# Kernel tuning notes

Hardware: AMD Instinct MI355X
Metric: run time of the kernel (lower is better)

## Reference

```python
import jax, jax.numpy as jnp
import numpy as np

K_NN = 4  # hard-coded k in get_graph_feature(x, k=4)


def _conv1(h, Wm, s, b):
    # 1x1 conv1d + folded-BN (scale/shift) + ReLU
    return jax.nn.relu(jnp.einsum('oc,bcn->bon', Wm, h) * s[:, None] + b[:, None])


def _conv2(h, Wm, s, b):
    # 1x1 conv2d + folded-BN + ReLU
    return jax.nn.relu(jnp.einsum('oc,bcnk->bonk', Wm, h) * s[:, None, None] + b[:, None, None])


def _forward(x, W_dup, s_dup, b_dup, W_c1, s_c1, b_c1,
             W2a, s2a, b2a, W2b, s2b, b2b, W2c, s2c, b2c,
             W3a, s3a, b3a, W3b, s3b, b3b, W4a, bias4a, W4b, bias4b):
    B = x.shape[0]
    h = _conv1(x, W_dup, s_dup, b_dup)           # (B,256,1024)
    h = h.reshape(B, 128, 2048)                  # duplicate points: (B,128,2048)
    h = _conv1(h, W_c1, s_c1, b_c1)              # (B,64,2048)
    g = jnp.max(h, axis=2, keepdims=True)        # max_pool1d over all 2048 -> (B,64,1)
    # knn on 64-d features: pairwise = -||xi-xj||^2, topk picks nearest (self included)
    xx = jnp.sum(h * h, axis=1, keepdims=True)   # (B,1,P)
    inner = -2.0 * jnp.einsum('bcn,bcm->bnm', h, h)
    pd = -xx - inner - jnp.swapaxes(xx, 1, 2)    # (B,P,P)
    idx = jax.lax.top_k(pd, K_NN)[1]             # (B,P,k)
    xt = jnp.swapaxes(h, 1, 2)                   # (B,P,C)
    nb = xt[jnp.arange(B)[:, None, None], idx]   # gather neighbors: (B,P,k,C)
    ctr = xt[:, :, None, :]
    feat = jnp.concatenate([nb - ctr, jnp.broadcast_to(ctr, nb.shape)], axis=-1)  # (B,P,k,2C)
    feat = jnp.transpose(feat, (0, 3, 1, 2))     # (B,128,P,k)
    feat = _conv2(feat, W2a, s2a, b2a)
    feat = _conv2(feat, W2b, s2b, b2b)
    feat = _conv2(feat, W2c, s2c, b2c)           # (B,64,P,k)
    local = jnp.max(feat, axis=3)                # max over k -> (B,64,P)
    g = _conv1(g, W3a, s3a, b3a)
    g = _conv1(g, W3b, s3b, b3b)                 # (B,128,1)
    final = jnp.concatenate([local, jnp.broadcast_to(g, (B, 128, local.shape[2]))], axis=1)  # (B,192,P)
    h4 = jax.nn.relu(jnp.einsum('oc,bcn->bon', W4a, final) + bias4a[:, None])  # (B,256,P)
    out = jnp.einsum('oc,bcn->bon', W4b, h4) + bias4b[:, None]                 # (B,3,P)
    return out


def setup_inputs() -> dict:
    key = jax.random.key(0)
    ks = list(jax.random.split(key, 30))
    W = lambda k, o, c: jax.random.normal(k, (o, c), jnp.float32) * 0.05
    sc = lambda k, c: 1.0 + 0.1 * jax.random.normal(k, (c,), jnp.float32)
    bs = lambda k, c: 0.1 * jax.random.normal(k, (c,), jnp.float32)
    return {
        'search_keypoint': jax.random.normal(ks[0], (8, 128, 1024), jnp.float32),
        'W_dup': W(ks[1], 256, 128), 's_dup': sc(ks[2], 256), 'b_dup': bs(ks[3], 256),
        'W_c1': W(ks[4], 64, 128), 's_c1': sc(ks[5], 64), 'b_c1': bs(ks[6], 64),
        'W2a': W(ks[7], 64, 128), 's2a': sc(ks[8], 64), 'b2a': bs(ks[9], 64),
        'W2b': W(ks[10], 64, 64), 's2b': sc(ks[11], 64), 'b2b': bs(ks[12], 64),
        'W2c': W(ks[13], 64, 64), 's2c': sc(ks[14], 64), 'b2c': bs(ks[15], 64),
        'W3a': W(ks[16], 128, 64), 's3a': sc(ks[17], 128), 'b3a': bs(ks[18], 128),
        'W3b': W(ks[19], 128, 128), 's3b': sc(ks[20], 128), 'b3b': bs(ks[21], 128),
        'W4a': W(ks[22], 256, 192), 'bias4a': bs(ks[23], 256),
        'W4b': W(ks[24], 3, 256), 'bias4b': bs(ks[25], 3),
    }


def reference(search_keypoint, W_dup, s_dup, b_dup, W_c1, s_c1, b_c1,
              W2a, s2a, b2a, W2b, s2b, b2b, W2c, s2c, b2c,
              W3a, s3a, b3a, W3b, s3b, b3b, W4a, bias4a, W4b, bias4b):
    return _forward(search_keypoint, W_dup, s_dup, b_dup, W_c1, s_c1, b_c1,
                    W2a, s2a, b2a, W2b, s2b, b2b, W2c, s2c, b2c,
                    W3a, s3a, b3a, W3b, s3b, b3b, W4a, bias4a, W4b, bias4b)
```

## Files before the change

kernel.cpp:

```cpp
#include <hip/hip_runtime.h>
#include <float.h>

typedef __attribute__((ext_vector_type(8))) short short8;
typedef __attribute__((ext_vector_type(4))) float f32x4;
typedef unsigned short u16;
typedef unsigned long long u64;

static constexpr size_t OFF_W     = 0;
static constexpr size_t OFF_YZ    = 131072;
static constexpr size_t OFF_Zf    = 1179648;
static constexpr size_t OFF_FEATR = 2228224;
static constexpr size_t OFF_FIN   = 6422528;
static constexpr size_t OFF_XX    = 9568256;
static constexpr size_t OFF_G     = 9584640;
static constexpr size_t OFF_G3BS  = 9617408;
static constexpr size_t WS_FLOATS = 9652736;

static constexpr size_t WO_DUP = 0;
static constexpr size_t WO_C1  = 32768;
static constexpr size_t WO_2A  = 40960;
static constexpr size_t WO_2B  = 49152;
static constexpr size_t WO_2C  = 53248;
static constexpr size_t WO_4A  = 57344;

__device__ __forceinline__ void gl_lds16(const void* g, void* l) {
    __builtin_amdgcn_global_load_lds(
        (const __attribute__((address_space(1))) void*)g,
        (__attribute__((address_space(3))) void*)l, 16, 0, 0);
}

__device__ __forceinline__ u16 f2bf(float x) {
    union { float f; unsigned int u; } v; v.f = x;
    unsigned int r = v.u + 0x7fffu + ((v.u >> 16) & 1u);
    return (u16)(r >> 16);
}
__device__ __forceinline__ float bf2f(u16 h) {
    union { unsigned int u; float f; } v; v.u = ((unsigned int)h) << 16;
    return v.f;
}
__device__ __forceinline__ void split2(float x, u16& h, u16& l) {
    h = f2bf(x);
    l = f2bf(x - bf2f(h));
}

__device__ __forceinline__ unsigned int fmap(float f) {
    unsigned int u = __float_as_uint(f);
    return u ^ ((unsigned int)((int)u >> 31) | 0x80000000u);
}
__device__ __forceinline__ u64 mkkey(float f, int m) {
    return ((u64)fmap(f) << 32) | (unsigned int)(2047 - m);
}
static __device__ __forceinline__ void ins4k(u64 k, u64 bk[4])
{
#pragma unroll
    for (int s = 0; s < 4; ++s) {
        bool better = k > bk[s];
        u64 t = bk[s];
        bk[s] = better ? k : bk[s];
        k = better ? t : k;
    }
}

__global__ __launch_bounds__(256) void wsplit(
    const float* W_dup, const float* W_c1, const float* W2a,
    const float* W2b, const float* W2c, const float* W4a,
    u16* whi, u16* wlo)
{
    int t = blockIdx.x * 256 + threadIdx.x;
    float v;
    if      (t < 40960) v = (t < 32768) ? W_dup[t] : W_c1[t - 32768];
    else if (t < 53248) v = (t < 49152) ? W2a[t - 40960] : W2b[t - 49152];
    else                v = (t < 57344) ? W2c[t - 53248] : W4a[t - 57344];
    u16 h, l; split2(v, h, l);
    whi[t] = h; wlo[t] = l;
}

__global__ __launch_bounds__(256) void tsplit_x(const float* x, u16* xthi, u16* xtlo)
{
    const int b = blockIdx.z, c0 = blockIdx.y * 64, n0 = blockIdx.x * 64;
    const int t = threadIdx.x;
    __shared__ float tile[64][65];
    const float* xb = x + ((size_t)b * 128 + c0) * 1024;
#pragma unroll
    for (int i = 0; i < 16; ++i) {
        int c = i * 4 + (t >> 6), n = t & 63;
        tile[c][n] = xb[(size_t)c * 1024 + n0 + n];
    }
    __syncthreads();
#pragma unroll
    for (int i = 0; i < 16; ++i) {
        int n = i * 4 + (t >> 6), c = t & 63;
        u16 h, l; split2(tile[c][n], h, l);
        const size_t o = ((size_t)b * 1024 + n0 + n) * 128 + c0 + c;
        xthi[o] = h; xtlo[o] = l;
    }
}

__global__ __launch_bounds__(256) void backbone(
    const u16* __restrict__ xthi, const u16* __restrict__ xtlo,
    const u16* __restrict__ whi, const u16* __restrict__ wlo,
    const float* __restrict__ s_dup, const float* __restrict__ b_dup,
    const float* __restrict__ s_c1, const float* __restrict__ b_c1,
    u16* __restrict__ h2thi, u16* __restrict__ h2tlo,
    float* __restrict__ xxb, float* __restrict__ gp,
    float* __restrict__ y, float* __restrict__ z)
{
    const int t = threadIdx.x;
    const int wu = t >> 6;
    const int lane = t & 63;
    const int j = lane & 15, q = lane >> 4;
    const int nb = blockIdx.x;
    const int b  = blockIdx.y;
    const int n0 = nb * 16;

    __shared__ __align__(16) u16 h1h[32 * 136], h1l[32 * 136];
    __shared__ __align__(16) u16 h2h[32 * 72],  h2l[32 * 72];
    __shared__ float xxp[2][2][16];
    __shared__ float gpart[2][64];

    {
        const size_t arow = ((size_t)b * 1024 + n0 + j) * 128;
        short8 ahv[4], alv[4];
#pragma unroll
        for (int ks = 0; ks < 4; ++ks) {
            ahv[ks] = *(const short8*)(xthi + arow + q * 8 + ks * 32);
            alv[ks] = *(const short8*)(xtlo + arow + q * 8 + ks * 32);
        }
        const u16* wdh = whi + WO_DUP;
        const u16* wdl = wlo + WO_DUP;
#pragma unroll
        for (int ci = 0; ci < 4; ++ci) {
            const int o = (wu * 4 + ci) * 16 + j;
            f32x4 acc = (f32x4){0.f, 0.f, 0.f, 0.f};
#pragma unroll
            for (int ks = 0; ks < 4; ++ks) {
                short8 bh = *(const short8*)(wdh + (size_t)o * 128 + q * 8 + ks * 32);
                short8 bl = *(const short8*)(wdl + (size_t)o * 128 + q * 8 + ks * 32);
                acc = __builtin_amdgcn_mfma_f32_16x16x32_bf16(ahv[ks], bh, acc, 0, 0, 0);
                acc = __builtin_amdgcn_mfma_f32_16x16x32_bf16(ahv[ks], bl, acc, 0, 0, 0);
                acc = __builtin_amdgcn_mfma_f32_16x16x32_bf16(alv[ks], bh, acc, 0, 0, 0);
            }
            const float sc = s_dup[o], bi = b_dup[o];
            const int lrbase = (j & 1) * 16;
            const int col = (wu * 4 + ci) * 8 + (j >> 1);
#pragma unroll
            for (int r = 0; r < 4; ++r) {
                float v = fmaxf(acc[r] * sc + bi, 0.f);
                u16 h, l; split2(v, h, l);
                const int lr = lrbase + q * 4 + r;
                h1h[lr * 136 + col] = h;
                h1l[lr * 136 + col] = l;
            }
        }
    }
    __syncthreads();

    {
        const int g = wu >> 1, ch = wu & 1;
        short8 ahv[4], alv[4];
#pragma unroll
        for (int ks = 0; ks < 4; ++ks) {
            ahv[ks] = *(const short8*)&h1h[(g * 16 + j) * 136 + q * 8 + ks * 32];
            alv[ks] = *(const short8*)&h1l[(g * 16 + j) * 136 + q * 8 + ks * 32];
        }
        const u16* wch = whi + WO_C1;
        const u16* wcl = wlo + WO_C1;
        float sq[4] = {0.f, 0.f, 0.f, 0.f};
        float cm[2];
#pragma unroll
        for (int ci = 0; ci < 2; ++ci) {
            const int o = (ch * 2 + ci) * 16 + j;
            f32x4 acc = (f32x4){0.f, 0.f, 0.f, 0.f};
#pragma unroll
            for (int ks = 0; ks < 4; ++ks) {
                short8 bh = *(const short8*)(wch + (size_t)o * 128 + q * 8 + ks * 32);
                short8 bl = *(const short8*)(wcl + (size_t)o * 128 + q * 8 + ks * 32);
                acc = __builtin_amdgcn_mfma_f32_16x16x32_bf16(ahv[ks], bh, acc, 0, 0, 0);
                acc = __builtin_amdgcn_mfma_f32_16x16x32_bf16(ahv[ks], bl, acc, 0, 0, 0);
                acc = __builtin_amdgcn_mfma_f32_16x16x32_bf16(alv[ks], bh, acc, 0, 0, 0);
            }
            const float sc = s_c1[o], bi = b_c1[o];
            float vmax = -FLT_MAX;
#pragma unroll
            for (int r = 0; r < 4; ++r) {
                float v = fmaxf(acc[r] * sc + bi, 0.f);
                sq[r] += v * v;
                vmax = fmaxf(vmax, v);
                u16 h, l; split2(v, h, l);
                const size_t R = (size_t)b * 2048 + g * 1024 + n0 + q * 4 + r;
                h2thi[R * 64 + o] = h;
                h2tlo[R * 64 + o] = l;
                const int lr = g * 16 + q * 4 + r;
                h2h[lr * 72 + o] = h;
                h2l[lr * 72 + o] = l;
            }
            cm[ci] = vmax;
        }
#pragma unroll
        for (int r = 0; r < 4; ++r) {
#pragma unroll
            for (int mask = 1; mask < 16; mask <<= 1)
                sq[r] += __shfl_xor(sq[r], mask, 64);
        }
        if (j == 0) {
#pragma unroll
            for (int r = 0; r < 4; ++r) xxp[g][ch][q * 4 + r] = sq[r];
        }
#pragma unroll
        for (int ci = 0; ci < 2; ++ci) {
            cm[ci] = fmaxf(cm[ci], __shfl_xor(cm[ci], 16, 64));
            cm[ci] = fmaxf(cm[ci], __shfl_xor(cm[ci], 32, 64));
        }
        if (q == 0) {
#pragma unroll
            for (int ci = 0; ci < 2; ++ci)
                gpart[g][(ch * 2 + ci) * 16 + j] = cm[ci];
        }
    }
    __syncthreads();

    if (t < 32) {
        const int g = t >> 4, i = t & 15;
        xxb[(size_t)b * 2048 + g * 1024 + n0 + i] = xxp[g][0][i] + xxp[g][1][i];
    }
    if (t >= 64 && t < 128) {
        const int c = t - 64;
        gp[((size_t)b * 64 + nb) * 64 + c] = fmaxf(gpart[0][c], gpart[1][c]);
    }

    {
        const int g = wu & 1, half = wu >> 1;
        short8 ahv[2], alv[2];
#pragma unroll
        for (int ks = 0; ks < 2; ++ks) {
            ahv[ks] = *(const short8*)&h2h[(g * 16 + j) * 72 + q * 8 + ks * 32];
            alv[ks] = *(const short8*)&h2l[(g * 16 + j) * 72 + q * 8 + ks * 32];
        }
        const u16* w2h = whi + WO_2A;
        const u16* w2l = wlo + WO_2A;
        float* dst = half ? z : y;
#pragma unroll
        for (int ci = 0; ci < 4; ++ci) {
            const int o = ci * 16 + j;
            f32x4 acc = (f32x4){0.f, 0.f, 0.f, 0.f};
#pragma unroll
            for (int ks = 0; ks < 2; ++ks) {
                short8 bh = *(const short8*)(w2h + (size_t)o * 128 + half * 64 + q * 8 + ks * 32);
                short8 bl = *(const short8*)(w2l + (size_t)o * 128 + half * 64 + q * 8 + ks * 32);
                acc = __builtin_amdgcn_mfma_f32_16x16x32_bf16(ahv[ks], bh, acc, 0, 0, 0);
                acc = __builtin_amdgcn_mfma_f32_16x16x32_bf16(ahv[ks], bl, acc, 0, 0, 0);
                acc = __builtin_amdgcn_mfma_f32_16x16x32_bf16(alv[ks], bh, acc, 0, 0, 0);
            }
#pragma unroll
            for (int r = 0; r < 4; ++r) {
                const size_t R = (size_t)b * 2048 + g * 1024 + n0 + q * 4 + r;
                dst[R * 64 + o] = acc[r];
            }
        }
    }
}

struct __align__(16) KBuf {
    u16 hi[4096];
    u16 lo[4096];
    float xm[64];
};

__global__ __launch_bounds__(256) void knn_topk(const u16* __restrict__ thi,
                                                const u16* __restrict__ tlo,
                                                const float* __restrict__ xx,
                                                u64* __restrict__ part)
{
    const int b    = blockIdx.z;
    const int mq   = blockIdx.y;
    const int t    = threadIdx.x;
    const int wu   = __builtin_amdgcn_readfirstlane(t >> 6);
    const int lane = t & 63;
    const int j    = lane & 15;
    const int q    = lane >> 4;
    const int nrow0 = blockIdx.x * 64 + wu * 16;

    const u16* th = thi + (size_t)b * 2048 * 64;
    const u16* tl = tlo + (size_t)b * 2048 * 64;
    const float* xb = xx + (size_t)b * 2048;

    __shared__ KBuf sb[2];

    const size_t arow = (size_t)(nrow0 + j) * 64;
    short8 ah0 = *(const short8*)(th + arow + q * 8);
    short8 ah1 = *(const short8*)(th + arow + 32 + q * 8);
    short8 al0 = *(const short8*)(tl + arow + q * 8);
    short8 al1 = *(const short8*)(tl + arow + 32 + q * 8);

    u64 bk[4][4];
#pragma unroll
    for (int r = 0; r < 4; ++r)
#pragma unroll
        for (int s = 0; s < 4; ++s) bk[r][s] = 0ull;

    const int mbeg = mq * 512;

#define KNN_STAGE(BUF, M0)                                                        \
    {                                                                             \
        const u16* sh = th + (size_t)((M0) + lane) * 64;                          \
        const u16* sl = tl + (size_t)((M0) + lane) * 64;                          \
        gl_lds16(sh + (2 * wu) * 8,     &sb[BUF].hi[(2 * wu) * 512]);             \
        gl_lds16(sh + (2 * wu + 1) * 8, &sb[BUF].hi[(2 * wu + 1) * 512]);         \
        gl_lds16(sl + (2 * wu) * 8,     &sb[BUF].lo[(2 * wu) * 512]);             \
        gl_lds16(sl + (2 * wu + 1) * 8, &sb[BUF].lo[(2 * wu + 1) * 512]);         \
        if (wu == 0 && lane < 16) gl_lds16(xb + (M0) + lane * 4, &sb[BUF].xm[0]); \
    }

    KNN_STAGE(0, mbeg)

    for (int tt = 0; tt < 8; ++tt) {
        __syncthreads();
        if (tt < 7) KNN_STAGE((tt + 1) & 1, mbeg + (tt + 1) * 64)
        const KBuf& bf = sb[tt & 1];
        const int m0 = mbeg + tt * 64;

        float pds[4][4];
#pragma unroll
        for (int sub = 0; sub < 4; ++sub) {
            const int ml = sub * 16 + j;
            short8 bh0 = *(const short8*)&bf.hi[(q) * 512 + ml * 8];
            short8 bh1 = *(const short8*)&bf.hi[(4 + q) * 512 + ml * 8];
            short8 bl0 = *(const short8*)&bf.lo[(q) * 512 + ml * 8];
            short8 bl1 = *(const short8*)&bf.lo[(4 + q) * 512 + ml * 8];
            const float xmv = bf.xm[ml];
            f32x4 accA = (f32x4){0.f, 0.f, 0.f, 0.f};
            f32x4 accB = (f32x4){0.f, 0.f, 0.f, 0.f};
            accA = __builtin_amdgcn_mfma_f32_16x16x32_bf16(ah0, bh0, accA, 0, 0, 0);
            accB = __builtin_amdgcn_mfma_f32_16x16x32_bf16(ah1, bh1, accB, 0, 0, 0);
            accA = __builtin_amdgcn_mfma_f32_16x16x32_bf16(ah0, bl0, accA, 0, 0, 0);
            accB = __builtin_amdgcn_mfma_f32_16x16x32_bf16(ah1, bl1, accB, 0, 0, 0);
            accA = __builtin_amdgcn_mfma_f32_16x16x32_bf16(al0, bh0, accA, 0, 0, 0);
            accB = __builtin_amdgcn_mfma_f32_16x16x32_bf16(al1, bh1, accB, 0, 0, 0);
            accA = __builtin_amdgcn_mfma_f32_16x16x32_bf16(al0, bl0, accA, 0, 0, 0);
            accB = __builtin_amdgcn_mfma_f32_16x16x32_bf16(al1, bl1, accB, 0, 0, 0);
#pragma unroll
            for (int r = 0; r < 4; ++r)
                pds[sub][r] = __builtin_fmaf(2.f, accA[r] + accB[r], -xmv);
        }

#pragma unroll
        for (int r = 0; r < 4; ++r) {
            float mx = fmaxf(fmaxf(pds[0][r], pds[1][r]), fmaxf(pds[2][r], pds[3][r]));
            if (fmap(mx) >= (unsigned int)(bk[r][3] >> 32)) {
#pragma unroll
                for (int sub = 0; sub < 4; ++sub) {
                    u64 key = mkkey(pds[sub][r], m0 + sub * 16 + j);
                    if (key > bk[r][3]) ins4k(key, bk[r]);
                }
            }
        }
    }
#undef KNN_STAGE

#pragma unroll
    for (int rr = 0; rr < 4; ++rr) {
#pragma unroll
        for (int mask = 1; mask < 16; mask <<= 1) {
            u64 pk[4];
#pragma unroll
            for (int s = 0; s < 4; ++s) pk[s] = __shfl_xor(bk[rr][s], mask, 64);
#pragma unroll
            for (int s = 0; s < 4; ++s) ins4k(pk[s], bk[rr]);
        }
    }
    if (j == 0) {
#pragma unroll
        for (int r = 0; r < 4; ++r) {
            const int nrow = nrow0 + q * 4 + r;
            u64* pp = part + (((size_t)b * 4 + mq) * 2048 + nrow) * 4;
            pp[0] = bk[r][0]; pp[1] = bk[r][1]; pp[2] = bk[r][2]; pp[3] = bk[r][3];
        }
    }
}

__global__ __launch_bounds__(128) void gconv_kernel(
    const float* __restrict__ gp,
    const float* __restrict__ W3a, const float* __restrict__ s3a, const float* __restrict__ b3a,
    const float* __restrict__ W3b, const float* __restrict__ s3b, const float* __restrict__ b3b,
    u16* __restrict__ g3bh, u16* __restrict__ g3bl)
{
    const int b = blockIdx.x;
    const int t = threadIdx.x;
    __shared__ float gl[64], ga[128];
    if (t < 64) {
        float m = -FLT_MAX;
        for (int s = 0; s < 64; ++s)
            m = fmaxf(m, gp[((size_t)b * 64 + s) * 64 + t]);
        gl[t] = m;
    }
    __syncthreads();
    float a = 0.f;
#pragma unroll
    for (int c = 0; c < 64; ++c) a += W3a[t * 64 + c] * gl[c];
    ga[t] = fmaxf(a * s3a[t] + b3a[t], 0.f);
    __syncthreads();
    float o = 0.f;
#pragma unroll
    for (int c = 0; c < 128; ++c) o += W3b[t * 128 + c] * ga[c];
    float v = fmaxf(o * s3b[t] + b3b[t], 0.f);
    u16 h, l; split2(v, h, l);
    g3bh[(size_t)b * 128 + t] = h;
    g3bl[(size_t)b * 128 + t] = l;
}

__global__ __launch_bounds__(256) void fused_edge(
    const u64* __restrict__ part,
    const float* __restrict__ y, const float* __restrict__ z,
    const float* __restrict__ s2a, const float* __restrict__ b2a,
    const u16* __restrict__ w2bh, const u16* __restrict__ w2bl,
    const float* __restrict__ s2b, const float* __restrict__ b2b,
    const u16* __restrict__ w2ch, const u16* __restrict__ w2cl,
    const float* __restrict__ s2c, const float* __restrict__ b2c,
    const u16* __restrict__ g3bh, const u16* __restrict__ g3bl,
    u16* __restrict__ finhi, u16* __restrict__ finlo)
{
    const int t = threadIdx.x;
    const int wu = t >> 6;
    const int lane = t & 63;
    const int j = lane & 15, q = lane >> 4;
    const int gb = blockIdx.x;
    const int b = gb >> 7;
    const int n0 = (gb & 127) * 16;

    __shared__ __align__(16) u16 plh[64 * 72];
    __shared__ __align__(16) u16 pll[64 * 72];
    __shared__ int sidx[64];

    if (lane < 4) {
        const int n = n0 + wu * 4 + lane;
        u64 fk[4] = {0ull, 0ull, 0ull, 0ull};
#pragma unroll
        for (int qt = 0; qt < 4; ++qt) {
            const u64* pp = part + (((size_t)b * 4 + qt) * 2048 + n) * 4;
#pragma unroll
            for (int s = 0; s < 4; ++s) ins4k(pp[s], fk);
        }
        int4 ii;
        ii.x = 2047 - (int)(fk[0] & 0x7ff);
        ii.y = 2047 - (int)(fk[1] & 0x7ff);
        ii.z = 2047 - (int)(fk[2] & 0x7ff);
        ii.w = 2047 - (int)(fk[3] & 0x7ff);
        *(int4*)&sidx[wu * 16 + lane * 4] = ii;
    }

    {
        const int row = lane >> 2;
        const int c0 = (lane & 3) * 16;
        const int id = sidx[wu * 16 + row];
        const int nfull = n0 + wu * 4 + (row >> 2);
        const float* yb = y + (size_t)b * 2048 * 64;
        const float* yi = yb + (size_t)id * 64;
        const float* yn = yb + (size_t)nfull * 64;
        const float* zn = z + ((size_t)b * 2048 + nfull) * 64;
        u16* oh = &plh[(wu * 16 + row) * 72 + c0];
        u16* ol = &pll[(wu * 16 + row) * 72 + c0];
#pragma unroll
        for (int cc = 0; cc < 16; cc += 4) {
            const int c = c0 + cc;
            float4 a  = *(const float4*)(yi + c);
            float4 bq = *(const float4*)(yn + c);
            float4 cq = *(const float4*)(zn + c);
            float4 sv = *(const float4*)(s2a + c);
            float4 bb = *(const float4*)(b2a + c);
            float v0 = fmaxf((a.x - bq.x + cq.x) * sv.x + bb.x, 0.f);
            float v1 = fmaxf((a.y - bq.y + cq.y) * sv.y + bb.y, 0.f);
            float v2 = fmaxf((a.z - bq.z + cq.z) * sv.z + bb.z, 0.f);
            float v3 = fmaxf((a.w - bq.w + cq.w) * sv.w + bb.w, 0.f);
            union { u16 u[4]; uint2 v; } ph, pl;
            split2(v0, ph.u[0], pl.u[0]);
            split2(v1, ph.u[1], pl.u[1]);
            split2(v2, ph.u[2], pl.u[2]);
            split2(v3, ph.u[3], pl.u[3]);
            *(uint2*)(oh + cc) = ph.v;
            *(uint2*)(ol + cc) = pl.v;
        }
    }

    {
        const int abase = (wu * 16 + j) * 72 + q * 8;
        short8 ah0 = *(const short8*)&plh[abase];
        short8 ah1 = *(const short8*)&plh[abase + 32];
        short8 al0 = *(const short8*)&pll[abase];
        short8 al1 = *(const short8*)&pll[abase + 32];
#pragma unroll
        for (int ct = 0; ct < 4; ++ct) {
            const int o = ct * 16 + j;
            short8 bh0 = *(const short8*)(w2bh + (size_t)o * 64 + q * 8);
            short8 bh1 = *(const short8*)(w2bh + (size_t)o * 64 + 32 + q * 8);
            short8 bl0 = *(const short8*)(w2bl + (size_t)o * 64 + q * 8);
            short8 bl1 = *(const short8*)(w2bl + (size_t)o * 64 + 32 + q * 8);
            f32x4 acc = (f32x4){0.f, 0.f, 0.f, 0.f};
            acc = __builtin_amdgcn_mfma_f32_16x16x32_bf16(ah0, bh0, acc, 0, 0, 0);
            acc = __builtin_amdgcn_mfma_f32_16x16x32_bf16(ah0, bl0, acc, 0, 0, 0);
            acc = __builtin_amdgcn_mfma_f32_16x16x32_bf16(al0, bh0, acc, 0, 0, 0);
            acc = __builtin_amdgcn_mfma_f32_16x16x32_bf16(ah1, bh1, acc, 0, 0, 0);
            acc = __builtin_amdgcn_mfma_f32_16x16x32_bf16(ah1, bl1, acc, 0, 0, 0);
            acc = __builtin_amdgcn_mfma_f32_16x16x32_bf16(al1, bh1, acc, 0, 0, 0);
            const float sc = s2b[o], bi = b2b[o];
#pragma unroll
            for (int r = 0; r < 4; ++r) {
                float v = fmaxf(acc[r] * sc + bi, 0.f);
                u16 h, l; split2(v, h, l);
                const int row = wu * 16 + q * 4 + r;
                plh[row * 72 + o] = h;
                pll[row * 72 + o] = l;
            }
        }
    }

    {
        const int abase = (wu * 16 + j) * 72 + q * 8;
        short8 ah0 = *(const short8*)&plh[abase];
        short8 ah1 = *(const short8*)&plh[abase + 32];
        short8 al0 = *(const short8*)&pll[abase];
        short8 al1 = *(const short8*)&pll[abase + 32];
        const size_t finrow = (size_t)b * 2048 + n0 + wu * 4 + q;
#pragma unroll
        for (int ct = 0; ct < 4; ++ct) {
            const int o = ct * 16 + j;
            short8 bh0 = *(const short8*)(w2ch + (size_t)o * 64 + q * 8);
            short8 bh1 = *(const short8*)(w2ch + (size_t)o * 64 + 32 + q * 8);
            short8 bl0 = *(const short8*)(w2cl + (size_t)o * 64 + q * 8);
            short8 bl1 = *(const short8*)(w2cl + (size_t)o * 64 + 32 + q * 8);
            f32x4 acc = (f32x4){0.f, 0.f, 0.f, 0.f};
            acc = __builtin_amdgcn_mfma_f32_16x16x32_bf16(ah0, bh0, acc, 0, 0, 0);
            acc = __builtin_amdgcn_mfma_f32_16x16x32_bf16(ah0, bl0, acc, 0, 0, 0);
            acc = __builtin_amdgcn_mfma_f32_16x16x32_bf16(al0, bh0, acc, 0, 0, 0);
            acc = __builtin_amdgcn_mfma_f32_16x16x32_bf16(ah1, bh1, acc, 0, 0, 0);
            acc = __builtin_amdgcn_mfma_f32_16x16x32_bf16(ah1, bl1, acc, 0, 0, 0);
            acc = __builtin_amdgcn_mfma_f32_16x16x32_bf16(al1, bh1, acc, 0, 0, 0);
            const float sc = s2c[o], bi = b2c[o];
            float m = -FLT_MAX;
#pragma unroll
            for (int r = 0; r < 4; ++r)
                m = fmaxf(m, fmaxf(acc[r] * sc + bi, 0.f));
            u16 h, l; split2(m, h, l);
            finhi[finrow * 192 + o] = h;
            finlo[finrow * 192 + o] = l;
        }

        const int r = lane >> 4;
        const int chunk = lane & 15;
        const size_t br = (size_t)b * 2048 + n0 + wu * 4 + r;
        short8 gh = *(const short8*)(g3bh + (size_t)b * 128 + chunk * 8);
        short8 glv = *(const short8*)(g3bl + (size_t)b * 128 + chunk * 8);
        *(short8*)(finhi + br * 192 + 64 + chunk * 8) = gh;
        *(short8*)(finlo + br * 192 + 64 + chunk * 8) = glv;
    }
}

__global__ __launch_bounds__(256) void conv_final(
    const u16* __restrict__ Whi, const u16* __restrict__ Wlo,
    const float* __restrict__ bias,
    const u16* __restrict__ Ahi, const u16* __restrict__ Alo,
    const float* __restrict__ W2, const float* __restrict__ bias2,
    float* __restrict__ out)
{
    const int t = threadIdx.x;
    const int wu = t >> 6;
    const int lane = t & 63;
    const int j = lane & 15, q = lane >> 4;
    const int n0g = blockIdx.x * 64 + wu * 16;

    short8 a_hi[6], a_lo[6];
    const u16* arow_h = Ahi + (size_t)(n0g + j) * 192 + q * 8;
    const u16* arow_l = Alo + (size_t)(n0g + j) * 192 + q * 8;
#pragma unroll
    for (int ks = 0; ks < 6; ++ks) {
        a_hi[ks] = *(const short8*)(arow_h + ks * 32);
        a_lo[ks] = *(const short8*)(arow_l + ks * 32);
    }

    float p[3][4];
#pragma unroll
    for (int oo = 0; oo < 3; ++oo)
#pragma unroll
        for (int r = 0; r < 4; ++r) p[oo][r] = 0.f;

#pragma unroll
    for (int ct = 0; ct < 16; ++ct) {
        const int o = ct * 16 + j;
        const u16* wr_h = Whi + (size_t)o * 192 + q * 8;
        const u16* wr_l = Wlo + (size_t)o * 192 + q * 8;
        f32x4 acc = (f32x4){0.f, 0.f, 0.f, 0.f};
#pragma unroll
        for (int ks = 0; ks < 6; ++ks) {
            short8 bh = *(const short8*)(wr_h + ks * 32);
            short8 bl = *(const short8*)(wr_l + ks * 32);
            acc = __builtin_amdgcn_mfma_f32_16x16x32_bf16(a_hi[ks], bh, acc, 0, 0, 0);
            acc = __builtin_amdgcn_mfma_f32_16x16x32_bf16(a_hi[ks], bl, acc, 0, 0, 0);
            acc = __builtin_amdgcn_mfma_f32_16x16x32_bf16(a_lo[ks], bh, acc, 0, 0, 0);
        }
        const float bi = bias[o];
        float w0 = W2[o], w1 = W2[256 + o], w2 = W2[512 + o];
#pragma unroll
        for (int r = 0; r < 4; ++r) {
            float v = fmaxf(acc[r] + bi, 0.f);
            p[0][r] += w0 * v;
            p[1][r] += w1 * v;
            p[2][r] += w2 * v;
        }
    }

#pragma unroll
    for (int oo = 0; oo < 3; ++oo)
#pragma unroll
        for (int r = 0; r < 4; ++r) {
#pragma unroll
            for (int mask = 1; mask < 16; mask <<= 1)
                p[oo][r] += __shfl_xor(p[oo][r], mask, 64);
        }
    if (j == 0) {
        const int row0 = n0g + q * 4;
        const int b = row0 >> 11;
#pragma unroll
        for (int r = 0; r < 4; ++r) {
            const int n = (row0 + r) & 2047;
#pragma unroll
            for (int oo = 0; oo < 3; ++oo)
                out[((size_t)b * 3 + oo) * 2048 + n] = p[oo][r] + bias2[oo];
        }
    }
}

extern "C" void kernel_launch(void* const* d_in, const int* in_sizes, int n_in,
                              void* d_out, int out_size, void* d_ws, size_t ws_size,
                              hipStream_t stream)
{
    const float* x     = (const float*)d_in[0];
    const float* W_dup = (const float*)d_in[1];
    const float* s_dup = (const float*)d_in[2];
    const float* b_dup = (const float*)d_in[3];
    const float* W_c1  = (const float*)d_in[4];
    const float* s_c1  = (const float*)d_in[5];
    const float* b_c1  = (const float*)d_in[6];
    const float* W2a   = (const float*)d_in[7];
    const float* s2a   = (const float*)d_in[8];
    const float* b2a   = (const float*)d_in[9];
    const float* W2b   = (const float*)d_in[10];
    const float* s2b   = (const float*)d_in[11];
    const float* b2b   = (const float*)d_in[12];
    const float* W2c   = (const float*)d_in[13];
    const float* s2c   = (const float*)d_in[14];
    const float* b2c   = (const float*)d_in[15];
    const float* W3a   = (const float*)d_in[16];
    const float* s3a   = (const float*)d_in[17];
    const float* b3a   = (const float*)d_in[18];
    const float* W3b   = (const float*)d_in[19];
    const float* s3b   = (const float*)d_in[20];
    const float* b3b   = (const float*)d_in[21];
    const float* W4a   = (const float*)d_in[22];
    const float* b4a   = (const float*)d_in[23];
    const float* W4b   = (const float*)d_in[24];
    const float* b4b   = (const float*)d_in[25];

    if (ws_size < WS_FLOATS * sizeof(float)) return;

    float* ws = (float*)d_ws;
    u16* whi   = (u16*)(ws + OFF_W);
    u16* wlo   = whi + 131072;
    u16* xthi  = (u16*)(ws + OFF_FEATR);
    u16* xtlo  = xthi + 1048576;
    u64* part  = (u64*)(ws + OFF_FEATR);
    float* y    = ws + OFF_YZ;
    float* z    = ws + OFF_Zf;
    u16* h2thi = (u16*)(ws + OFF_FIN);
    u16* h2tlo = h2thi + 1048576;
    u16* finhi  = (u16*)(ws + OFF_FIN);
    u16* finlo  = finhi + 3145728;
    float* xxb  = ws + OFF_XX;
    float* gp   = ws + OFF_G;
    u16* g3bh   = (u16*)(ws + OFF_G3BS);
    u16* g3bl   = g3bh + 1024;
    float* out  = (float*)d_out;

    wsplit<<<416, 256, 0, stream>>>(W_dup, W_c1, W2a, W2b, W2c, W4a, whi, wlo);
    tsplit_x<<<dim3(16, 2, 8), 256, 0, stream>>>(x, xthi, xtlo);
    backbone<<<dim3(64, 8), 256, 0, stream>>>(
        xthi, xtlo, whi, wlo, s_dup, b_dup, s_c1, b_c1,
        h2thi, h2tlo, xxb, gp, y, z);
    gconv_kernel<<<8, 128, 0, stream>>>(gp, W3a, s3a, b3a, W3b, s3b, b3b, g3bh, g3bl);
    knn_topk<<<dim3(32, 4, 8), 256, 0, stream>>>(h2thi, h2tlo, xxb, part);
    fused_edge<<<1024, 256, 0, stream>>>(
        part, y, z, s2a, b2a,
        whi + WO_2B, wlo + WO_2B, s2b, b2b,
        whi + WO_2C, wlo + WO_2C, s2c, b2c,
        g3bh, g3bl, finhi, finlo);
    conv_final<<<256, 256, 0, stream>>>(
        whi + WO_4A, wlo + WO_4A, b4a, finhi, finlo, W4b, b4b, out);
}
```

Baseline: 268.0 us.

## Halve knn column splits and shrink edge/final kernels to single-wave blocks

The knn top-k kernel now splits the candidate range into 2 halves of 1024 columns instead of 4 quarters of 512. Each block therefore runs 16 staged tiles, and the per-row merge in fused_edge reads only two partial lists. fused_edge and conv_final are changed from 4-wave 256-thread blocks to single-wave 64-thread blocks, with four times as many blocks and smaller shared buffers. This reduces partial-result traffic and merge work and gives finer-grained scheduling. The cost is fewer knn blocks (512) and longer serial loops per block, which may leave CUs idle.

```diff
diff --git a/kernel.cpp b/kernel.cpp
--- a/kernel.cpp
+++ b/kernel.cpp
@@ -272,7 +272,7 @@
                                                 u64* __restrict__ part)
 {
     const int b    = blockIdx.z;
-    const int mq   = blockIdx.y;
+    const int mh   = blockIdx.y;
     const int t    = threadIdx.x;
     const int wu   = __builtin_amdgcn_readfirstlane(t >> 6);
     const int lane = t & 63;
@@ -298,7 +298,7 @@
 #pragma unroll
         for (int s = 0; s < 4; ++s) bk[r][s] = 0ull;
 
-    const int mbeg = mq * 512;
+    const int mbeg = mh * 1024;
 
 #define KNN_STAGE(BUF, M0)                                                        \
     {                                                                             \
@@ -313,9 +313,9 @@
 
     KNN_STAGE(0, mbeg)
 
-    for (int tt = 0; tt < 8; ++tt) {
+    for (int tt = 0; tt < 16; ++tt) {
         __syncthreads();
-        if (tt < 7) KNN_STAGE((tt + 1) & 1, mbeg + (tt + 1) * 64)
+        if (tt < 15) KNN_STAGE((tt + 1) & 1, mbeg + (tt + 1) * 64)
         const KBuf& bf = sb[tt & 1];
         const int m0 = mbeg + tt * 64;
 
@@ -372,7 +372,7 @@
 #pragma unroll
         for (int r = 0; r < 4; ++r) {
             const int nrow = nrow0 + q * 4 + r;
-            u64* pp = part + (((size_t)b * 4 + mq) * 2048 + nrow) * 4;
+            u64* pp = part + (((size_t)b * 2 + mh) * 2048 + nrow) * 4;
             pp[0] = bk[r][0]; pp[1] = bk[r][1]; pp[2] = bk[r][2]; pp[3] = bk[r][3];
         }
     }
@@ -408,7 +408,7 @@
     g3bl[(size_t)b * 128 + t] = l;
 }
 
-__global__ __launch_bounds__(256) void fused_edge(
+__global__ __launch_bounds__(64) void fused_edge(
     const u64* __restrict__ part,
     const float* __restrict__ y, const float* __restrict__ z,
     const float* __restrict__ s2a, const float* __restrict__ b2a,
@@ -419,24 +419,22 @@
     const u16* __restrict__ g3bh, const u16* __restrict__ g3bl,
     u16* __restrict__ finhi, u16* __restrict__ finlo)
 {
-    const int t = threadIdx.x;
-    const int wu = t >> 6;
-    const int lane = t & 63;
+    const int lane = threadIdx.x & 63;
     const int j = lane & 15, q = lane >> 4;
     const int gb = blockIdx.x;
-    const int b = gb >> 7;
-    const int n0 = (gb & 127) * 16;
-
-    __shared__ __align__(16) u16 plh[64 * 72];
-    __shared__ __align__(16) u16 pll[64 * 72];
-    __shared__ int sidx[64];
+    const int b = gb >> 9;
+    const int n0 = (gb & 511) * 4;
+
+    __shared__ __align__(16) u16 plh[16 * 72];
+    __shared__ __align__(16) u16 pll[16 * 72];
+    __shared__ int sidx[16];
 
     if (lane < 4) {
-        const int n = n0 + wu * 4 + lane;
+        const int n = n0 + lane;
         u64 fk[4] = {0ull, 0ull, 0ull, 0ull};
 #pragma unroll
-        for (int qt = 0; qt < 4; ++qt) {
-            const u64* pp = part + (((size_t)b * 4 + qt) * 2048 + n) * 4;
+        for (int qt = 0; qt < 2; ++qt) {
+            const u64* pp = part + (((size_t)b * 2 + qt) * 2048 + n) * 4;
 #pragma unroll
             for (int s = 0; s < 4; ++s) ins4k(pp[s], fk);
         }
@@ -445,20 +443,20 @@
         ii.y = 2047 - (int)(fk[1] & 0x7ff);
         ii.z = 2047 - (int)(fk[2] & 0x7ff);
         ii.w = 2047 - (int)(fk[3] & 0x7ff);
-        *(int4*)&sidx[wu * 16 + lane * 4] = ii;
+        *(int4*)&sidx[lane * 4] = ii;
     }
 
     {
         const int row = lane >> 2;
         const int c0 = (lane & 3) * 16;
-        const int id = sidx[wu * 16 + row];
-        const int nfull = n0 + wu * 4 + (row >> 2);
+        const int id = sidx[row];
+        const int nfull = n0 + (row >> 2);
         const float* yb = y + (size_t)b * 2048 * 64;
         const float* yi = yb + (size_t)id * 64;
         const float* yn = yb + (size_t)nfull * 64;
         const float* zn = z + ((size_t)b * 2048 + nfull) * 64;
-        u16* oh = &plh[(wu * 16 + row) * 72 + c0];
-        u16* ol = &pll[(wu * 16 + row) * 72 + c0];
+        u16* oh = &plh[row * 72 + c0];
+        u16* ol = &pll[row * 72 + c0];
 #pragma unroll
         for (int cc = 0; cc < 16; cc += 4) {
             const int c = c0 + cc;
@@ -482,7 +480,7 @@
     }
 
     {
-        const int abase = (wu * 16 + j) * 72 + q * 8;
+        const int abase = j * 72 + q * 8;
         short8 ah0 = *(const short8*)&plh[abase];
         short8 ah1 = *(const short8*)&plh[abase + 32];
         short8 al0 = *(const short8*)&pll[abase];
@@ -506,7 +504,7 @@
             for (int r = 0; r < 4; ++r) {
                 float v = fmaxf(acc[r] * sc + bi, 0.f);
                 u16 h, l; split2(v, h, l);
-                const int row = wu * 16 + q * 4 + r;
+                const int row = q * 4 + r;
                 plh[row * 72 + o] = h;
                 pll[row * 72 + o] = l;
             }
@@ -514,12 +512,12 @@
     }
 
     {
-        const int abase = (wu * 16 + j) * 72 + q * 8;
+        const int abase = j * 72 + q * 8;
         short8 ah0 = *(const short8*)&plh[abase];
         short8 ah1 = *(const short8*)&plh[abase + 32];
         short8 al0 = *(const short8*)&pll[abase];
         short8 al1 = *(const short8*)&pll[abase + 32];
-        const size_t finrow = (size_t)b * 2048 + n0 + wu * 4 + q;
+        const size_t finrow = (size_t)b * 2048 + n0 + q;
 #pragma unroll
         for (int ct = 0; ct < 4; ++ct) {
             const int o = ct * 16 + j;
@@ -546,7 +544,7 @@
 
         const int r = lane >> 4;
         const int chunk = lane & 15;
-        const size_t br = (size_t)b * 2048 + n0 + wu * 4 + r;
+        const size_t br = (size_t)b * 2048 + n0 + r;
         short8 gh = *(const short8*)(g3bh + (size_t)b * 128 + chunk * 8);
         short8 glv = *(const short8*)(g3bl + (size_t)b * 128 + chunk * 8);
         *(short8*)(finhi + br * 192 + 64 + chunk * 8) = gh;
@@ -554,18 +552,16 @@
     }
 }
 
-__global__ __launch_bounds__(256) void conv_final(
+__global__ __launch_bounds__(64) void conv_final(
     const u16* __restrict__ Whi, const u16* __restrict__ Wlo,
     const float* __restrict__ bias,
     const u16* __restrict__ Ahi, const u16* __restrict__ Alo,
     const float* __restrict__ W2, const float* __restrict__ bias2,
     float* __restrict__ out)
 {
-    const int t = threadIdx.x;
-    const int wu = t >> 6;
-    const int lane = t & 63;
+    const int lane = threadIdx.x & 63;
     const int j = lane & 15, q = lane >> 4;
-    const int n0g = blockIdx.x * 64 + wu * 16;
+    const int n0g = blockIdx.x * 16;
 
     short8 a_hi[6], a_lo[6];
     const u16* arow_h = Ahi + (size_t)(n0g + j) * 192 + q * 8;
@@ -685,12 +681,12 @@
         xthi, xtlo, whi, wlo, s_dup, b_dup, s_c1, b_c1,
         h2thi, h2tlo, xxb, gp, y, z);
     gconv_kernel<<<8, 128, 0, stream>>>(gp, W3a, s3a, b3a, W3b, s3b, b3b, g3bh, g3bl);
-    knn_topk<<<dim3(32, 4, 8), 256, 0, stream>>>(h2thi, h2tlo, xxb, part);
-    fused_edge<<<1024, 256, 0, stream>>>(
+    knn_topk<<<dim3(32, 2, 8), 256, 0, stream>>>(h2thi, h2tlo, xxb, part);
+    fused_edge<<<4096, 64, 0, stream>>>(
         part, y, z, s2a, b2a,
         whi + WO_2B, wlo + WO_2B, s2b, b2b,
         whi + WO_2C, wlo + WO_2C, s2c, b2c,
         g3bh, g3bl, finhi, finlo);
-    conv_final<<<256, 256, 0, stream>>>(
+    conv_final<<<1024, 64, 0, stream>>>(
         whi + WO_4A, wlo + WO_4A, b4a, finhi, finlo, W4b, b4b, out);
 }
```

After: 261.1 us. -2.6%, faster.
